# Performance work log

Hardware: AMD Instinct MI355X
Metric: run time of the kernel (lower is better)

Reference implementation:

```python
import jax, jax.numpy as jnp
import numpy as np

N = 100000   # nodes
E = 1200000  # edges
H = 64       # hidden_channels
G = 256      # graphs in the batch
C_IN = 1
C_OUT = 2


def setup_inputs() -> dict:
    key = jax.random.key(0)
    ks = jax.random.split(key, 16)

    def lin_w(k, fan_in, fan_out):
        bound = 1.0 / np.sqrt(fan_in)
        return jax.random.uniform(k, (fan_in, fan_out), jnp.float32, -bound, bound)

    def lin_b(k, fan_in, fan_out):
        bound = 1.0 / np.sqrt(fan_in)
        return jax.random.uniform(k, (fan_out,), jnp.float32, -bound, bound)

    return {
        "x": jax.random.normal(ks[0], (N, C_IN), jnp.float32),
        "edge_index": jax.random.randint(ks[1], (2, E), 0, N),
        "batch": jnp.sort(jax.random.randint(ks[2], (N,), 0, G)),
        "edge_weight": jax.random.uniform(ks[3], (E,), jnp.float32),
        # GraphConv 1: lin_rel (bias) + lin_root (no bias)
        "W1_rel": lin_w(ks[4], C_IN, H), "b1": lin_b(ks[5], C_IN, H), "W1_root": lin_w(ks[6], C_IN, H),
        # GraphConv 2
        "W2_rel": lin_w(ks[7], H, H), "b2": lin_b(ks[8], H, H), "W2_root": lin_w(ks[9], H, H),
        # GraphConv 3
        "W3_rel": lin_w(ks[10], H, H), "b3": lin_b(ks[11], H, H), "W3_root": lin_w(ks[12], H, H),
        # head
        "W_lin": lin_w(ks[13], H, C_OUT), "b_lin": lin_b(ks[14], H, C_OUT),
    }


def _graph_conv(x, src, dst, ew, W_rel, b_rel, W_root):
    # message: edge_weight * x[src]; aggr='add' to dst; then lin_rel(aggr) + lin_root(x)
    m = x[src] * ew[:, None]                                    # [E, C]
    agg = jax.ops.segment_sum(m, dst, num_segments=x.shape[0])  # [N, C]
    return agg @ W_rel + b_rel + x @ W_root


def reference(x, edge_index, batch, edge_weight,
              W1_rel, b1, W1_root, W2_rel, b2, W2_root, W3_rel, b3, W3_root,
              W_lin, b_lin):
    src, dst = edge_index[0], edge_index[1]
    h = jax.nn.relu(_graph_conv(x, src, dst, edge_weight, W1_rel, b1, W1_root))
    h = jax.nn.relu(_graph_conv(h, src, dst, edge_weight, W2_rel, b2, W2_root))
    h = _graph_conv(h, src, dst, edge_weight, W3_rel, b3, W3_root)
    # global mean pool over graph id
    sums = jax.ops.segment_sum(h, batch, num_segments=G)                        # [G, H]
    cnts = jax.ops.segment_sum(jnp.ones((h.shape[0],), h.dtype), batch, num_segments=G)
    pooled = sums / jnp.maximum(cnts, 1.0)[:, None]
    # dropout is identity in eval mode
    return pooled @ W_lin + b_lin                                               # [G, 2]
```

## Files before the change

kernel.cpp:

```cpp
#include <hip/hip_runtime.h>


#define BKT_SHIFT 7
#define BKT_SZ    128
#define NBK_MAX   1024
#define CHUNK     4096

static __device__ __forceinline__ float4 ld4(const float* p) {
    return *reinterpret_cast<const float4*>(p);
}
static __device__ __forceinline__ float rdlane(float v, int i) {
    return __int_as_float(__builtin_amdgcn_readlane(__float_as_int(v), i));
}

__global__ void k_small(const float* __restrict__ W3_rel, const float* __restrict__ b3,
                        const float* __restrict__ W3_root, const float* __restrict__ W_lin,
                        float4* __restrict__ MC4, float* __restrict__ b3W,
                        int* __restrict__ zbase, int zwords)
{
    int gt = blockIdx.x * 256 + threadIdx.x;
    for (int i = gt; i < zwords; i += gridDim.x * 256) zbase[i] = 0;

    if (blockIdx.x == 0) {
        int t = threadIdx.x;
        if (t < 64) {
            float sr0 = 0.f, sr1 = 0.f, so0 = 0.f, so1 = 0.f;
            for (int k = 0; k < 64; ++k) {
                float wl0 = W_lin[k * 2 + 0], wl1 = W_lin[k * 2 + 1];
                sr0 += W3_rel[t * 64 + k] * wl0;
                sr1 += W3_rel[t * 64 + k] * wl1;
                so0 += W3_root[t * 64 + k] * wl0;
                so1 += W3_root[t * 64 + k] * wl1;
            }
            MC4[t] = make_float4(sr0, sr1, so0, so1);
        }
        if (t < 2) {
            float s = 0.f;
            for (int k = 0; k < 64; ++k) s += b3[k] * W_lin[k * 2 + t];
            b3W[t] = s;
        }
    }
}

__global__ __launch_bounds__(256) void k_hist2(const int* __restrict__ dst,
                                               int* __restrict__ bcnt, int E, int NBK)
{
    __shared__ int lh[NBK_MAX];
    for (int i = threadIdx.x; i < NBK; i += 256) lh[i] = 0;
    __syncthreads();
    int e0 = blockIdx.x * CHUNK;
#pragma unroll
    for (int k = 0; k < 16; ++k) {
        int e = e0 + k * 256 + threadIdx.x;
        if (e < E) atomicAdd(&lh[dst[e] >> BKT_SHIFT], 1);
    }
    __syncthreads();
    for (int i = threadIdx.x; i < NBK; i += 256) {
        int v = lh[i];
        if (v) atomicAdd(&bcnt[i], v);
    }
}

__global__ __launch_bounds__(256) void k_scanb(const int* __restrict__ bcnt,
                                               int* __restrict__ bb, int NBK)
{
    __shared__ int tmp[256];
    int t = threadIdx.x;
    int loc[4]; int s = 0;
#pragma unroll
    for (int u = 0; u < 4; ++u) {
        int idx = t * 4 + u;
        loc[u] = (idx < NBK) ? bcnt[idx] : 0;
        s += loc[u];
    }
    tmp[t] = s;
    __syncthreads();
    for (int off = 1; off < 256; off <<= 1) {
        int v = (t >= off) ? tmp[t - off] : 0;
        __syncthreads();
        tmp[t] += v;
        __syncthreads();
    }
    int run = tmp[t] - s;
#pragma unroll
    for (int u = 0; u < 4; ++u) {
        int idx = t * 4 + u;
        if (idx < NBK) bb[idx] = run;
        run += loc[u];
    }
    if (t == 255) bb[NBK] = run;
}

__global__ __launch_bounds__(256) void k_scatter2(const int* __restrict__ src,
                                                  const int* __restrict__ dst,
                                                  const float* __restrict__ ew,
                                                  const int* __restrict__ bb,
                                                  int* __restrict__ cursor,
                                                  int2* __restrict__ ebuf, int E, int NBK)
{
    __shared__ int lofs[NBK_MAX + 1];
    __shared__ int rcur[NBK_MAX];
    __shared__ int delta[NBK_MAX];
    __shared__ int2 stage[CHUNK];
    __shared__ unsigned short sbkt[CHUNK];
    __shared__ int tmp[256];

    const int t = threadIdx.x;
    const int e0 = blockIdx.x * CHUNK;
    const int cnt = min(CHUNK, E - e0);

    for (int i = t; i < NBK; i += 256) lofs[i] = 0;
    __syncthreads();

    int   myb[16];
    int   mypk[16];
    float myw[16];
#pragma unroll
    for (int k = 0; k < 16; ++k) {
        int e = e0 + k * 256 + t;
        myb[k] = -1;
        if (e < E) {
            int d = dst[e];
            int b = d >> BKT_SHIFT;
            myb[k]  = b;
            mypk[k] = ((d & (BKT_SZ - 1)) << 17) | src[e];
            myw[k]  = ew[e];
            atomicAdd(&lofs[b], 1);
        }
    }
    __syncthreads();

    int loc[4]; int s = 0;
#pragma unroll
    for (int u = 0; u < 4; ++u) {
        int idx = t * 4 + u;
        loc[u] = (idx < NBK) ? lofs[idx] : 0;
        s += loc[u];
    }
    tmp[t] = s;
    __syncthreads();
    for (int off = 1; off < 256; off <<= 1) {
        int v = (t >= off) ? tmp[t - off] : 0;
        __syncthreads();
        tmp[t] += v;
        __syncthreads();
    }
    int run = tmp[t] - s;
#pragma unroll
    for (int u = 0; u < 4; ++u) {
        int idx = t * 4 + u;
        if (idx < NBK) { lofs[idx] = run; rcur[idx] = run; }
        run += loc[u];
    }
    if (t == 255) lofs[NBK] = run;
    __syncthreads();

    for (int b = t; b < NBK; b += 256) {
        int c = lofs[b + 1] - lofs[b];
        if (c > 0) {
            int g0 = atomicAdd(&cursor[b], c);
            delta[b] = bb[b] + g0 - lofs[b];
        }
    }
    __syncthreads();

#pragma unroll
    for (int k = 0; k < 16; ++k) {
        if (myb[k] >= 0) {
            int p = atomicAdd(&rcur[myb[k]], 1);
            stage[p] = make_int2(mypk[k], __float_as_int(myw[k]));
            sbkt[p]  = (unsigned short)myb[k];
        }
    }
    __syncthreads();

    for (int i = t; i < cnt; i += 256) {
        int b = sbkt[i];
        ebuf[delta[b] + i] = stage[i];
    }
}

__global__ __launch_bounds__(256) void k_sort3a(const int2* __restrict__ ebuf,
                                                const int* __restrict__ bb,
                                                const float* __restrict__ x,
                                                int* __restrict__ rowptr,
                                                int2* __restrict__ csr,
                                                float2* __restrict__ axn,
                                                int N, int E)
{
    __shared__ int cnt_[BKT_SZ];
    __shared__ int sc[BKT_SZ];
    __shared__ int base_[BKT_SZ];
    __shared__ int cur_[BKT_SZ];
    __shared__ float a1[BKT_SZ];

    const int t = threadIdx.x;
    const int bk = blockIdx.x;
    if (t < BKT_SZ) { cnt_[t] = 0; a1[t] = 0.f; }
    __syncthreads();

    const int beg = bb[bk], end = bb[bk + 1];
    for (int i = beg + t; i < end; i += 256) {
        int dl = ebuf[i].x >> 17;
        atomicAdd(&cnt_[dl], 1);
    }
    __syncthreads();

    if (t < BKT_SZ) sc[t] = cnt_[t];
    __syncthreads();
    for (int off = 1; off < BKT_SZ; off <<= 1) {
        int v = (t < BKT_SZ && t >= off) ? sc[t - off] : 0;
        __syncthreads();
        if (t < BKT_SZ) sc[t] += v;
        __syncthreads();
    }
    if (t < BKT_SZ) {
        base_[t] = sc[t] - cnt_[t];
        cur_[t] = 0;
        int n = bk * BKT_SZ + t;
        if (n < N) rowptr[n] = beg + base_[t];
    }
    if (bk == 0 && t == 0) rowptr[N] = E;
    __syncthreads();

    for (int i = beg + t; i < end; i += 256) {
        int2 pw = ebuf[i];
        int dl = pw.x >> 17;
        int s_ = pw.x & 0x1FFFF;
        int pos = beg + base_[dl] + atomicAdd(&cur_[dl], 1);
        csr[pos] = make_int2(s_, pw.y);
        atomicAdd(&a1[dl], __int_as_float(pw.y) * x[s_]);
    }
    __syncthreads();

    int n = bk * BKT_SZ + t;
    if (t < BKT_SZ && n < N) axn[n] = make_float2(a1[t], x[n]);
}

__global__ __launch_bounds__(256) void k_agg2n(const int2* __restrict__ csr,
                                               const int* __restrict__ rowptr,
                                               const float2* __restrict__ axn,
                                               const int* __restrict__ batch,
                                               const float* __restrict__ W1_rel,
                                               const float* __restrict__ b1,
                                               const float* __restrict__ W1_root,
                                               const float* __restrict__ W2_rel,
                                               const float* __restrict__ W2_root,
                                               const float* __restrict__ b2,
                                               const float* __restrict__ MCf,
                                               float2* __restrict__ z01,
                                               float* __restrict__ gacc,
                                               int N, int G)
{
    __shared__ float T[BKT_SZ * 65];
    __shared__ float bins[256 * 3];

    const int t = threadIdx.x;
    const int bk = blockIdx.x;
    const int n0 = bk * BKT_SZ;
    const int lane = t & 63;
    const int wave = t >> 6;

    for (int i = t; i < 3 * G; i += 256) bins[i] = 0.f;

    const float wrel = W1_rel[lane], wroot = W1_root[lane], bj = b1[lane];

    int nn = n0 + wave * 32 + lane;
    int rp = 0;
    if (lane <= 32) rp = rowptr[min(nn, N)];

    for (int i = 0; i < 32; ++i) {
        int nl = wave * 32 + i;
        int b  = __builtin_amdgcn_readlane(rp, i);
        int en = __builtin_amdgcn_readlane(rp, i + 1);
        float acc = 0.f;
        for (int base = b; base < en; base += 64) {
            int e = base + lane;
            float wv = 0.f;
            float2 ax = make_float2(0.f, 0.f);
            if (e < en) {
                int2 sw = csr[e];
                wv = __int_as_float(sw.y);
                ax = axn[sw.x];
            }
            int cntm = min(en - base, 64);
#pragma unroll 4
            for (int j = 0; j < cntm; ++j) {
                float wj = rdlane(wv, j);
                float aj = rdlane(ax.x, j);
                float xj = rdlane(ax.y, j);
                float h = fmaxf(fmaf(aj, wrel, fmaf(xj, wroot, bj)), 0.f);
                acc = fmaf(wj, h, acc);
            }
        }
        T[nl * 65 + lane] = acc;
    }
    __syncthreads();

    const int g  = (t >> 7) & 1;
    const int hs = __builtin_amdgcn_readfirstlane((t >> 6) & 1);
    const int nl = g * 64 + lane;
    const int n  = n0 + nl;
    float2 ax = (n < N) ? axn[n] : make_float2(0.f, 0.f);

    float4 acc[8];
#pragma unroll
    for (int q = 0; q < 8; ++q) acc[q] = make_float4(0.f, 0.f, 0.f, 0.f);

    const float* Asr = &T[nl * 65];

    for (int c = 0; c < 8; ++c) {
        float a_[8];
#pragma unroll
        for (int i = 0; i < 8; ++i) a_[i] = Asr[c * 8 + i];
#pragma unroll
        for (int i = 0; i < 8; ++i) {
            const float* wr = &W2_rel[(size_t)(c * 8 + i) * 64 + hs * 32];
#pragma unroll
            for (int q = 0; q < 8; ++q) {
                float4 w = ld4(wr + q * 4);
                acc[q].x = fmaf(a_[i], w.x, acc[q].x);
                acc[q].y = fmaf(a_[i], w.y, acc[q].y);
                acc[q].z = fmaf(a_[i], w.z, acc[q].z);
                acc[q].w = fmaf(a_[i], w.w, acc[q].w);
            }
        }
    }

    for (int c = 0; c < 8; ++c) {
        int k0 = c * 8;
        float4 w1ra = ld4(&W1_rel[k0]),  w1rb = ld4(&W1_rel[k0 + 4]);
        float4 w1oa = ld4(&W1_root[k0]), w1ob = ld4(&W1_root[k0 + 4]);
        float4 b1a  = ld4(&b1[k0]),      b1b  = ld4(&b1[k0 + 4]);
        float hk[8];
        hk[0] = fmaxf(fmaf(ax.x, w1ra.x, fmaf(ax.y, w1oa.x, b1a.x)), 0.f);
        hk[1] = fmaxf(fmaf(ax.x, w1ra.y, fmaf(ax.y, w1oa.y, b1a.y)), 0.f);
        hk[2] = fmaxf(fmaf(ax.x, w1ra.z, fmaf(ax.y, w1oa.z, b1a.z)), 0.f);
        hk[3] = fmaxf(fmaf(ax.x, w1ra.w, fmaf(ax.y, w1oa.w, b1a.w)), 0.f);
        hk[4] = fmaxf(fmaf(ax.x, w1rb.x, fmaf(ax.y, w1ob.x, b1b.x)), 0.f);
        hk[5] = fmaxf(fmaf(ax.x, w1rb.y, fmaf(ax.y, w1ob.y, b1b.y)), 0.f);
        hk[6] = fmaxf(fmaf(ax.x, w1rb.z, fmaf(ax.y, w1ob.z, b1b.z)), 0.f);
        hk[7] = fmaxf(fmaf(ax.x, w1rb.w, fmaf(ax.y, w1ob.w, b1b.w)), 0.f);
#pragma unroll
        for (int i = 0; i < 8; ++i) {
            const float* wo = &W2_root[(size_t)(k0 + i) * 64 + hs * 32];
#pragma unroll
            for (int q = 0; q < 8; ++q) {
                float4 w = ld4(wo + q * 4);
                acc[q].x = fmaf(hk[i], w.x, acc[q].x);
                acc[q].y = fmaf(hk[i], w.y, acc[q].y);
                acc[q].z = fmaf(hk[i], w.z, acc[q].z);
                acc[q].w = fmaf(hk[i], w.w, acc[q].w);
            }
        }
    }

    float z0 = 0.f, z1 = 0.f, z2 = 0.f, z3 = 0.f;
    const float* b2h = &b2[hs * 32];
#pragma unroll
    for (int q = 0; q < 8; ++q) {
        float4 bq = ld4(b2h + q * 4);
        int jb = hs * 32 + q * 4;
        float h2;
        h2 = fmaxf(acc[q].x + bq.x, 0.f);
        { const float* m = &MCf[(jb + 0) * 4];
          z0 = fmaf(h2, m[0], z0); z1 = fmaf(h2, m[1], z1);
          z2 = fmaf(h2, m[2], z2); z3 = fmaf(h2, m[3], z3); }
        h2 = fmaxf(acc[q].y + bq.y, 0.f);
        { const float* m = &MCf[(jb + 1) * 4];
          z0 = fmaf(h2, m[0], z0); z1 = fmaf(h2, m[1], z1);
          z2 = fmaf(h2, m[2], z2); z3 = fmaf(h2, m[3], z3); }
        h2 = fmaxf(acc[q].z + bq.z, 0.f);
        { const float* m = &MCf[(jb + 2) * 4];
          z0 = fmaf(h2, m[0], z0); z1 = fmaf(h2, m[1], z1);
          z2 = fmaf(h2, m[2], z2); z3 = fmaf(h2, m[3], z3); }
        h2 = fmaxf(acc[q].w + bq.w, 0.f);
        { const float* m = &MCf[(jb + 3) * 4];
          z0 = fmaf(h2, m[0], z0); z1 = fmaf(h2, m[1], z1);
          z2 = fmaf(h2, m[2], z2); z3 = fmaf(h2, m[3], z3); }
    }

    __syncthreads();
    float* zs = T;
    *reinterpret_cast<float4*>(&zs[(nl * 2 + hs) * 4]) = make_float4(z0, z1, z2, z3);
    __syncthreads();
    if (hs == 0 && n < N) {
        float4 p0 = *reinterpret_cast<float4*>(&zs[(nl * 2 + 0) * 4]);
        float4 p1 = *reinterpret_cast<float4*>(&zs[(nl * 2 + 1) * 4]);
        z01[n] = make_float2(p0.x + p1.x, p0.y + p1.y);
        int bg = batch[n];
        atomicAdd(&bins[bg * 3 + 0], p0.z + p1.z);
        atomicAdd(&bins[bg * 3 + 1], p0.w + p1.w);
        atomicAdd(&bins[bg * 3 + 2], 1.0f);
    }
    __syncthreads();
    for (int i = t; i < 3 * G; i += 256) {
        float v = bins[i];
        if (v != 0.f) {
            int gg = i / 3, c = i % 3;
            atomicAdd(&gacc[gg * 5 + 2 + c], v);
        }
    }
}

__global__ __launch_bounds__(256) void k_poole(const int2* __restrict__ csr,
                                               const int* __restrict__ rowptr,
                                               const int* __restrict__ batch,
                                               const float2* __restrict__ z01,
                                               float* __restrict__ gacc, int N, int G)
{
    __shared__ float lds[2 * 256];
    for (int i = threadIdx.x; i < 2 * G; i += 256) lds[i] = 0.f;
    __syncthreads();

    int gt = blockIdx.x * 256 + threadIdx.x;
    int n = gt >> 2, p = gt & 3;
    if (n < N) {
        int b = rowptr[n], en = rowptr[n + 1];
        float s0 = 0.f, s1 = 0.f;
        for (int e = b + p; e < en; e += 4) {
            int2 sw = csr[e];
            float w = __int_as_float(sw.y);
            float2 zz = z01[sw.x];
            s0 = fmaf(w, zz.x, s0);
            s1 = fmaf(w, zz.y, s1);
        }
        s0 += __shfl_xor(s0, 1);
        s0 += __shfl_xor(s0, 2);
        s1 += __shfl_xor(s1, 1);
        s1 += __shfl_xor(s1, 2);
        if (p == 0) {
            int bg = batch[n];
            atomicAdd(&lds[bg * 2 + 0], s0);
            atomicAdd(&lds[bg * 2 + 1], s1);
        }
    }
    __syncthreads();
    for (int i = threadIdx.x; i < 2 * G; i += 256) {
        float v = lds[i];
        if (v != 0.f) atomicAdd(&gacc[(i >> 1) * 5 + (i & 1)], v);
    }
}

__global__ void k_final(const float* __restrict__ gacc, const float* __restrict__ b3W,
                        const float* __restrict__ b_lin, float* __restrict__ out, int G)
{
    int t = blockIdx.x * blockDim.x + threadIdx.x;
    if (t < G * 2) {
        int g = t >> 1, c = t & 1;
        float cnt = gacc[g * 5 + 4];
        float s = gacc[g * 5 + c] + gacc[g * 5 + 2 + c] + cnt * b3W[c];
        out[t] = s / fmaxf(cnt, 1.f) + b_lin[c];
    }
}

extern "C" void kernel_launch(void* const* d_in, const int* in_sizes, int n_in,
                              void* d_out, int out_size, void* d_ws, size_t ws_size,
                              hipStream_t stream)
{
    const float* x       = (const float*)d_in[0];
    const int*   ei      = (const int*)  d_in[1];
    const int*   batch   = (const int*)  d_in[2];
    const float* ew      = (const float*)d_in[3];
    const float* W1_rel  = (const float*)d_in[4];
    const float* b1      = (const float*)d_in[5];
    const float* W1_root = (const float*)d_in[6];
    const float* W2_rel  = (const float*)d_in[7];
    const float* b2      = (const float*)d_in[8];
    const float* W2_root = (const float*)d_in[9];
    const float* W3_rel  = (const float*)d_in[10];
    const float* b3      = (const float*)d_in[11];
    const float* W3_root = (const float*)d_in[12];
    const float* W_lin   = (const float*)d_in[13];
    const float* b_lin   = (const float*)d_in[14];
    float* out = (float*)d_out;

    const int N = in_sizes[0];
    const int E = in_sizes[3];
    const int G = out_size / 2;
    const int NBK = (N + BKT_SZ - 1) >> BKT_SHIFT;
    const int EB  = (E + CHUNK - 1) / CHUNK;
    const int* src = ei;
    const int* dst = ei + E;

    char* wsb = (char*)d_ws;
    size_t o = 0;
    auto take = [&](size_t bytes) -> char* {
        char* p = wsb + o;
        o += (bytes + 15) & ~(size_t)15;
        return p;
    };
    int*    cursor = (int*)   take((size_t)NBK * 4);
    int*    bcnt   = (int*)   take((size_t)NBK * 4);
    float*  gacc   = (float*) take((size_t)G * 5 * 4);
    size_t  zero_bytes = o;
    int*    bb     = (int*)   take((size_t)(NBK + 1) * 4);
    int*    rowptr = (int*)   take((size_t)(N + 1) * 4);
    int2*   ebuf   = (int2*)  take((size_t)E * 8);
    int2*   csr    = (int2*)  take((size_t)E * 8);
    float2* axn    = (float2*)take((size_t)N * 8);
    float2* z01    = (float2*)take((size_t)N * 8);
    float4* MC4    = (float4*)take(64 * 16);
    float*  b3W    = (float*) take(4 * 4);

    const int zwords = (int)(zero_bytes / 4);

    hipLaunchKernelGGL(k_small, dim3(8), dim3(256), 0, stream,
                       W3_rel, b3, W3_root, W_lin, MC4, b3W,
                       (int*)d_ws, zwords);

    hipLaunchKernelGGL(k_hist2, dim3(EB), dim3(256), 0, stream, dst, bcnt, E, NBK);
    hipLaunchKernelGGL(k_scanb, dim3(1), dim3(256), 0, stream, bcnt, bb, NBK);
    hipLaunchKernelGGL(k_scatter2, dim3(EB), dim3(256), 0, stream,
                       src, dst, ew, bb, cursor, ebuf, E, NBK);
    hipLaunchKernelGGL(k_sort3a, dim3(NBK), dim3(256), 0, stream,
                       ebuf, bb, x, rowptr, csr, axn, N, E);

    hipLaunchKernelGGL(k_agg2n, dim3(NBK), dim3(256), 0, stream,
                       csr, rowptr, axn, batch, W1_rel, b1, W1_root,
                       W2_rel, W2_root, b2, (const float*)MC4,
                       z01, gacc, N, G);

    hipLaunchKernelGGL(k_poole, dim3(((size_t)N * 4 + 255) / 256), dim3(256), 0, stream,
                       csr, rowptr, batch, z01, gacc, N, G);

    hipLaunchKernelGGL(k_final, dim3((G * 2 + 255) / 256), dim3(256), 0, stream,
                       gacc, b3W, b_lin, out, G);
}
```

Baseline: 147.0 us.

## Process bucket edges in flat 64-edge chunks with segmented LDS accumulation

```diff
diff --git a/kernel.cpp b/kernel.cpp
--- a/kernel.cpp
+++ b/kernel.cpp
@@ -228,7 +228,7 @@
         int dl = pw.x >> 17;
         int s_ = pw.x & 0x1FFFF;
         int pos = beg + base_[dl] + atomicAdd(&cur_[dl], 1);
-        csr[pos] = make_int2(s_, pw.y);
+        csr[pos] = make_int2((dl << 17) | s_, pw.y);
         atomicAdd(&a1[dl], __int_as_float(pw.y) * x[s_]);
     }
     __syncthreads();
@@ -238,9 +238,9 @@
 }
 
 __global__ __launch_bounds__(256) void k_agg2n(const int2* __restrict__ csr,
-                                               const int* __restrict__ rowptr,
                                                const float2* __restrict__ axn,
                                                const int* __restrict__ batch,
+                                               const int* __restrict__ bb,
                                                const float* __restrict__ W1_rel,
                                                const float* __restrict__ b1,
                                                const float* __restrict__ W1_root,
@@ -261,39 +261,41 @@
     const int lane = t & 63;
     const int wave = t >> 6;
 
+    for (int i = t; i < BKT_SZ * 65; i += 256) T[i] = 0.f;
     for (int i = t; i < 3 * G; i += 256) bins[i] = 0.f;
 
     const float wrel = W1_rel[lane], wroot = W1_root[lane], bj = b1[lane];
-
-    int nn = n0 + wave * 32 + lane;
-    int rp = 0;
-    if (lane <= 32) rp = rowptr[min(nn, N)];
-
-    for (int i = 0; i < 32; ++i) {
-        int nl = wave * 32 + i;
-        int b  = __builtin_amdgcn_readlane(rp, i);
-        int en = __builtin_amdgcn_readlane(rp, i + 1);
+    const int beg = bb[bk], end = bb[bk + 1];
+    __syncthreads();
+
+    for (int base = beg + wave * 64; base < end; base += 256) {
+        int e = base + lane;
+        int pk = 0;
+        float wv = 0.f, av = 0.f, xv = 0.f;
+        if (e < end) {
+            int2 sw = csr[e];
+            pk = sw.x;
+            wv = __int_as_float(sw.y);
+            float2 ax = axn[sw.x & 0x1FFFF];
+            av = ax.x; xv = ax.y;
+        }
+        int m = min(end - base, 64);
+        int cur_dl = -1;
         float acc = 0.f;
-        for (int base = b; base < en; base += 64) {
-            int e = base + lane;
-            float wv = 0.f;
-            float2 ax = make_float2(0.f, 0.f);
-            if (e < en) {
-                int2 sw = csr[e];
-                wv = __int_as_float(sw.y);
-                ax = axn[sw.x];
+        for (int j = 0; j < m; ++j) {
+            int dlj = __builtin_amdgcn_readlane(pk, j) >> 17;
+            float wj = rdlane(wv, j);
+            float aj = rdlane(av, j);
+            float xj = rdlane(xv, j);
+            if (dlj != cur_dl) {
+                if (cur_dl >= 0) atomicAdd(&T[cur_dl * 65 + lane], acc);
+                cur_dl = dlj;
+                acc = 0.f;
             }
-            int cntm = min(en - base, 64);
-#pragma unroll 4
-            for (int j = 0; j < cntm; ++j) {
-                float wj = rdlane(wv, j);
-                float aj = rdlane(ax.x, j);
-                float xj = rdlane(ax.y, j);
-                float h = fmaxf(fmaf(aj, wrel, fmaf(xj, wroot, bj)), 0.f);
-                acc = fmaf(wj, h, acc);
-            }
-        }
-        T[nl * 65 + lane] = acc;
+            float h = fmaxf(fmaf(aj, wrel, fmaf(xj, wroot, bj)), 0.f);
+            acc = fmaf(wj, h, acc);
+        }
+        if (cur_dl >= 0) atomicAdd(&T[cur_dl * 65 + lane], acc);
     }
     __syncthreads();
 
@@ -421,7 +423,7 @@
         for (int e = b + p; e < en; e += 4) {
             int2 sw = csr[e];
             float w = __int_as_float(sw.y);
-            float2 zz = z01[sw.x];
+            float2 zz = z01[sw.x & 0x1FFFF];
             s0 = fmaf(w, zz.x, s0);
             s1 = fmaf(w, zz.y, s1);
         }
@@ -517,7 +519,7 @@
                        ebuf, bb, x, rowptr, csr, axn, N, E);
 
     hipLaunchKernelGGL(k_agg2n, dim3(NBK), dim3(256), 0, stream,
-                       csr, rowptr, axn, batch, W1_rel, b1, W1_root,
+                       csr, axn, batch, bb, W1_rel, b1, W1_root,
                        W2_rel, W2_root, b2, (const float*)MC4,
                        z01, gacc, N, G);
 
```

Result: slower. 161.6 us (+9.9%).
